# Performance work log

Hardware: AMD Instinct MI355X
Metric: run time of the kernel (lower is better)

The kernel has to match this reference:

```python
import jax, jax.numpy as jnp
import numpy as np

N, E, C_IN, C_OUT = 50000, 800000, 64, 64
BN_EPS = 1e-5


def _batchnorm(h, gamma, beta):
    # Training-mode BatchNorm1d: batch statistics over dim 0, biased variance.
    mean = h.mean(axis=0)
    var = h.var(axis=0)  # ddof=0, matches PyTorch normalization stats
    return gamma * (h - mean) * jax.lax.rsqrt(var + BN_EPS) + beta


def setup_inputs() -> dict:
    key = jax.random.key(0)
    ks = jax.random.split(key, 6)
    x = jax.random.normal(ks[0], (N, C_IN), dtype=jnp.float32)
    edge_index = jax.random.randint(ks[1], (2, E), 0, N, dtype=jnp.int32)
    edge_weight = jax.random.uniform(ks[2], (E,), dtype=jnp.float32)
    s1 = 1.0 / np.sqrt(C_IN).astype(np.float32)
    s2 = 1.0 / np.sqrt(2 * C_IN).astype(np.float32)
    pool_W = jax.random.uniform(ks[3], (C_IN, C_IN), jnp.float32, -s1, s1)
    pool_b = jnp.zeros((C_IN,), jnp.float32)
    final_W = jax.random.uniform(ks[4], (2 * C_IN, C_OUT), jnp.float32, -s2, s2)
    final_b = jnp.zeros((C_OUT,), jnp.float32)
    return {
        "x": x,
        "edge_index": edge_index,
        "edge_weight": edge_weight,
        "pool_W": pool_W,
        "pool_b": pool_b,
        "bn_pool_gamma": jnp.ones((C_IN,), jnp.float32),
        "bn_pool_beta": jnp.zeros((C_IN,), jnp.float32),
        "final_W": final_W,
        "final_b": final_b,
        "bn_final_gamma": jnp.ones((C_OUT,), jnp.float32),
        "bn_final_beta": jnp.zeros((C_OUT,), jnp.float32),
        "coef": jnp.float32(0.5),
    }


def reference(x, edge_index, edge_weight, pool_W, pool_b, bn_pool_gamma,
              bn_pool_beta, final_W, final_b, bn_final_gamma, bn_final_beta,
              coef):
    src, dst = edge_index[0], edge_index[1]
    # gather src node features, scale by edge weight  -> [E, C_IN]
    edge_feat = x[src] * (1.0 + coef * edge_weight[:, None])
    pooled = edge_feat @ pool_W + pool_b              # [E, C_IN]
    pooled = jax.nn.relu(_batchnorm(pooled, bn_pool_gamma, bn_pool_beta))
    # scatter-max into destination nodes; empty segments -> 0 (pooled >= 0)
    agg = jax.ops.segment_max(pooled, dst, num_segments=x.shape[0])
    agg = jnp.maximum(agg, 0.0)                       # fill -inf (empty) with 0
    h = jnp.concatenate([x, agg], axis=-1) @ final_W + final_b  # [N, C_OUT]
    h = _batchnorm(h, bn_final_gamma, bn_final_beta)
    return jax.nn.relu(h)
```

## Files before the change

### kernel.cpp

```cpp
#include <hip/hip_runtime.h>
#include <hip/hip_fp16.h>
#include <math.h>
#include <float.h>

#define BN_EPS 1e-5f
#define SLOTS 64
#define SB 256


typedef __attribute__((ext_vector_type(8))) short bf16x8;
typedef __attribute__((ext_vector_type(4))) float f32x4;

__device__ inline unsigned short f2bf(float f) {
    unsigned u = __float_as_uint(f);
    return (unsigned short)((u + 0x7fffu + ((u >> 16) & 1u)) >> 16);
}
__device__ inline float bf2f(unsigned short h) {
    return __uint_as_float(((unsigned)h) << 16);
}

__global__ __launch_bounds__(256, 4) void k_scatter_gemm(
        const int* __restrict__ src, const int* __restrict__ dst,
        const float* __restrict__ w, const float* __restrict__ coef_p,
        int* __restrict__ cnt, unsigned* __restrict__ csr, int E,
        const float* __restrict__ x, const float* __restrict__ W,
        unsigned short* __restrict__ ybf, int nrows, int gemmGrid) {
    __shared__ unsigned short Wt[64 * 72];
    if (blockIdx.x < SB) {
        const float coef = *coef_p;
        const int tid = blockIdx.x * 256 + threadIdx.x;
        const int stride4 = SB * 256 * 4;
        for (int base = tid * 4; base < E; base += stride4) {
            if (base + 3 < E) {
                int4   s4 = *(const int4*)(src + base);
                int4   d4 = *(const int4*)(dst + base);
                float4 w4 = *(const float4*)(w + base);
                int sn[4] = {s4.x, s4.y, s4.z, s4.w};
                int dn[4] = {d4.x, d4.y, d4.z, d4.w};
                float wv[4] = {w4.x, w4.y, w4.z, w4.w};
                unsigned hs[4];
                int pos[4];
#pragma unroll
                for (int j = 0; j < 4; ++j) {
                    float s = fmaf(coef, wv[j], 1.0f);
                    hs[j] = (unsigned)__half_as_ushort(__float2half(s));
                    pos[j] = atomicAdd(&cnt[dn[j]], 1);
                }
#pragma unroll
                for (int j = 0; j < 4; ++j)
                    if (pos[j] < SLOTS)
                        csr[(size_t)dn[j] * SLOTS + pos[j]] =
                            ((unsigned)sn[j] << 16) | hs[j];
            } else {
                for (int i = base; i < E; ++i) {
                    int sn = src[i], tn = dst[i];
                    float s = fmaf(coef, w[i], 1.0f);
                    unsigned hs = (unsigned)__half_as_ushort(__float2half(s));
                    int pos = atomicAdd(&cnt[tn], 1);
                    if (pos < SLOTS)
                        csr[(size_t)tn * SLOTS + pos] = ((unsigned)sn << 16) | hs;
                }
            }
        }
        return;
    }
    const int bid = blockIdx.x - SB;
    for (int i = threadIdx.x; i < 64 * 64; i += 256) {
        int k = i >> 6, n = i & 63;
        Wt[n * 72 + k] = f2bf(W[i]);
    }
    __syncthreads();
    const int lane = threadIdx.x & 63;
    const int wave = threadIdx.x >> 6;
    const int quad = lane >> 4;
    const int ln = lane & 15;
    bf16x8 Bf[2][4];
#pragma unroll
    for (int kc = 0; kc < 2; ++kc)
#pragma unroll
        for (int ct = 0; ct < 4; ++ct)
            Bf[kc][ct] = *(const bf16x8*)&Wt[(ct * 16 + ln) * 72 + kc * 32 + quad * 8];
    const int T = (nrows + 15) >> 4;
    const int gw = bid * 4 + wave;
    const int nw = gemmGrid * 4;
    for (int t = gw; t < T; t += nw) {
        const int row = t * 16 + ln;
        bf16x8 af[2];
        if (row < nrows) {
            const float* xr = x + (size_t)row * 64;
#pragma unroll
            for (int kc = 0; kc < 2; ++kc) {
                float4 p = *(const float4*)(xr + kc * 32 + quad * 8);
                float4 q = *(const float4*)(xr + kc * 32 + quad * 8 + 4);
                bf16x8 a;
                a[0] = (short)f2bf(p.x); a[1] = (short)f2bf(p.y);
                a[2] = (short)f2bf(p.z); a[3] = (short)f2bf(p.w);
                a[4] = (short)f2bf(q.x); a[5] = (short)f2bf(q.y);
                a[6] = (short)f2bf(q.z); a[7] = (short)f2bf(q.w);
                af[kc] = a;
            }
        } else {
            bf16x8 z;
#pragma unroll
            for (int j = 0; j < 8; ++j) z[j] = 0;
            af[0] = z; af[1] = z;
        }
        f32x4 acc[4];
#pragma unroll
        for (int ct = 0; ct < 4; ++ct) { acc[ct][0]=0.f; acc[ct][1]=0.f; acc[ct][2]=0.f; acc[ct][3]=0.f; }
#pragma unroll
        for (int ct = 0; ct < 4; ++ct) {
            acc[ct] = __builtin_amdgcn_mfma_f32_16x16x32_bf16(af[0], Bf[0][ct], acc[ct], 0, 0, 0);
            acc[ct] = __builtin_amdgcn_mfma_f32_16x16x32_bf16(af[1], Bf[1][ct], acc[ct], 0, 0, 0);
        }
#pragma unroll
        for (int r = 0; r < 4; ++r) {
            int ro = t * 16 + quad * 4 + r;
            if (ro < nrows) {
#pragma unroll
                for (int ct = 0; ct < 4; ++ct)
                    ybf[(size_t)ro * 64 + ct * 16 + ln] = f2bf(acc[ct][r]);
            }
        }
    }
}

__global__ __launch_bounds__(256) void k_gather_max(const unsigned short* __restrict__ ybf,
                             const unsigned* __restrict__ csr, const int* __restrict__ cnt,
                             float* __restrict__ M, float* __restrict__ partials, int nrows) {
    int t = blockIdx.x * blockDim.x + threadIdx.x;
    int node = t >> 4;
    int sub = threadIdx.x & 15;
    int rg = threadIdx.x >> 4;
    int c0 = sub * 4;
    size_t base = (size_t)node * SLOTS;
    int dg = 0;
    if (node < nrows) { dg = cnt[node]; if (dg > SLOTS) dg = SLOTS; }
    float m0 = -FLT_MAX, m1 = -FLT_MAX, m2 = -FLT_MAX, m3 = -FLT_MAX;
    float s1[4] = {0, 0, 0, 0}, s2[4] = {0, 0, 0, 0};
    for (int k0 = 0; k0 < dg; k0 += 16) {
        int kk = k0 + sub;
        unsigned pk = (kk < dg) ? csr[base + kk] : 0u;
        int cnt16 = dg - k0; if (cnt16 > 16) cnt16 = 16;
        if (cnt16 == 16) {
            ushort4 uv[16];
            float sv[16];
#pragma unroll
            for (int j = 0; j < 16; ++j) {
                unsigned r = (unsigned)__shfl((int)pk, j, 16);
                sv[j] = __half2float(__ushort_as_half((unsigned short)(r & 0xffffu)));
                uv[j] = *(const ushort4*)&ybf[(size_t)(r >> 16) * 64 + c0];
            }
#pragma unroll
            for (int j = 0; j < 16; ++j) {
                float v0 = sv[j] * bf2f(uv[j].x), v1 = sv[j] * bf2f(uv[j].y);
                float v2 = sv[j] * bf2f(uv[j].z), v3 = sv[j] * bf2f(uv[j].w);
                m0 = fmaxf(m0, v0); s1[0] += v0; s2[0] = fmaf(v0, v0, s2[0]);
                m1 = fmaxf(m1, v1); s1[1] += v1; s2[1] = fmaf(v1, v1, s2[1]);
                m2 = fmaxf(m2, v2); s1[2] += v2; s2[2] = fmaf(v2, v2, s2[2]);
                m3 = fmaxf(m3, v3); s1[3] += v3; s2[3] = fmaf(v3, v3, s2[3]);
            }
        } else {
            for (int j = 0; j < cnt16; ++j) {
                unsigned r = (unsigned)__shfl((int)pk, j, 16);
                int sn = r >> 16;
                float sv = __half2float(__ushort_as_half((unsigned short)(r & 0xffffu)));
                ushort4 uv = *(const ushort4*)&ybf[(size_t)sn * 64 + c0];
                float v0 = sv * bf2f(uv.x), v1 = sv * bf2f(uv.y);
                float v2 = sv * bf2f(uv.z), v3 = sv * bf2f(uv.w);
                m0 = fmaxf(m0, v0); s1[0] += v0; s2[0] = fmaf(v0, v0, s2[0]);
                m1 = fmaxf(m1, v1); s1[1] += v1; s2[1] = fmaf(v1, v1, s2[1]);
                m2 = fmaxf(m2, v2); s1[2] += v2; s2[2] = fmaf(v2, v2, s2[2]);
                m3 = fmaxf(m3, v3); s1[3] += v3; s2[3] = fmaf(v3, v3, s2[3]);
            }
        }
    }
    if (node < nrows)
        *(float4*)&M[(size_t)node * 64 + c0] = make_float4(m0, m1, m2, m3);
    __shared__ float red[16][68];
#pragma unroll
    for (int j = 0; j < 4; ++j) red[rg][c0 + j] = s1[j];
    __syncthreads();
    if (rg == 0) {
#pragma unroll
        for (int j = 0; j < 4; ++j) {
            float tt = 0.0f;
            for (int r = 0; r < 16; ++r) tt += red[r][c0 + j];
            partials[(size_t)blockIdx.x * 128 + c0 + j] = tt;
        }
    }
    __syncthreads();
#pragma unroll
    for (int j = 0; j < 4; ++j) red[rg][c0 + j] = s2[j];
    __syncthreads();
    if (rg == 0) {
#pragma unroll
        for (int j = 0; j < 4; ++j) {
            float tt = 0.0f;
            for (int r = 0; r < 16; ++r) tt += red[r][c0 + j];
            partials[(size_t)blockIdx.x * 128 + 64 + c0 + j] = tt;
        }
    }
}

__global__ __launch_bounds__(256) void k_red1(const float* __restrict__ partials, int P,
                                              float* __restrict__ p2) {
    int c = threadIdx.x & 127;
    int half = threadIdx.x >> 7;
    float acc = 0.0f;
    for (int r = blockIdx.x * 2 + half; r < P; r += 256)
        acc += partials[(size_t)r * 128 + c];
    __shared__ float sh[256];
    sh[threadIdx.x] = acc;
    __syncthreads();
    if (half == 0) p2[(size_t)blockIdx.x * 128 + c] = sh[c] + sh[128 + c];
}

__global__ __launch_bounds__(1024) void k_red2(const float* __restrict__ p2,
                             const float* __restrict__ pool_b, const float* __restrict__ gamma,
                             const float* __restrict__ beta, float invE,
                             float* __restrict__ coef) {
    int c = threadIdx.x & 127;
    int seg = threadIdx.x >> 7;
    float acc = 0.0f;
    for (int r = seg; r < 128; r += 8) acc += p2[(size_t)r * 128 + c];
    __shared__ float red[8][128];
    red[seg][c] = acc;
    __syncthreads();
    if (seg == 0) {
        float tt = 0.0f;
#pragma unroll
        for (int s = 0; s < 8; ++s) tt += red[s][c];
        red[0][c] = tt;
    }
    __syncthreads();
    if (threadIdx.x < 64) {
        int c0 = threadIdx.x;
        float S1 = red[0][c0], S2 = red[0][64 + c0];
        float s1 = S1 * invE;
        float b = pool_b[c0];
        float mean = s1 + b;
        float ex2 = S2 * invE + 2.0f * b * s1 + b * b;
        float var = ex2 - mean * mean;
        float a = gamma[c0] * rsqrtf(var + BN_EPS);
        coef[c0] = a;
        coef[64 + c0] = beta[c0] - a * s1;
    }
}

__global__ __launch_bounds__(1024) void k_red2f(const float* __restrict__ p2,
                             const float* __restrict__ gamma, const float* __restrict__ beta,
                             float invN, float* __restrict__ coef) {
    int c = threadIdx.x & 127;
    int seg = threadIdx.x >> 7;
    float acc = 0.0f;
    for (int r = seg; r < 128; r += 8) acc += p2[(size_t)r * 128 + c];
    __shared__ float red[8][128];
    red[seg][c] = acc;
    __syncthreads();
    if (seg == 0) {
        float tt = 0.0f;
#pragma unroll
        for (int s = 0; s < 8; ++s) tt += red[s][c];
        red[0][c] = tt;
    }
    __syncthreads();
    if (threadIdx.x < 64) {
        int c0 = threadIdx.x;
        float mean = red[0][c0] * invN;
        float var = red[0][64 + c0] * invN - mean * mean;
        float a = gamma[c0] * rsqrtf(var + BN_EPS);
        coef[c0] = a;
        coef[64 + c0] = beta[c0] - a * mean;
    }
}

__global__ __launch_bounds__(256, 2) void k_final_gemm(const float* __restrict__ x,
                             const float* __restrict__ M, const float* __restrict__ coef,
                             const float* __restrict__ W, const float* __restrict__ b,
                             float* __restrict__ h, float* __restrict__ partials, int nrows) {
    __shared__ unsigned short Wt[64 * 136];
    __shared__ float hp[128];
    for (int i = threadIdx.x; i < 128 * 64; i += 256) {
        int k = i >> 6, n = i & 63;
        Wt[n * 136 + k] = f2bf(W[i]);
    }
    if (threadIdx.x < 128) hp[threadIdx.x] = 0.0f;
    __syncthreads();
    const int lane = threadIdx.x & 63;
    const int wave = threadIdx.x >> 6;
    const int quad = lane >> 4;
    const int ln = lane & 15;
    bf16x8 Bf[4][4];
#pragma unroll
    for (int kc = 0; kc < 4; ++kc)
#pragma unroll
        for (int ct = 0; ct < 4; ++ct)
            Bf[kc][ct] = *(const bf16x8*)&Wt[(ct * 16 + ln) * 136 + kc * 32 + quad * 8];
    float bias[4];
#pragma unroll
    for (int ct = 0; ct < 4; ++ct) bias[ct] = b[ct * 16 + ln];
    float ca[2][8], cd[2][8];
#pragma unroll
    for (int g = 0; g < 2; ++g) {
        int ch = g * 32 + quad * 8;
#pragma unroll
        for (int j = 0; j < 8; ++j) {
            ca[g][j] = coef[ch + j];
            cd[g][j] = coef[64 + ch + j];
        }
    }
    float ls1[4] = {0, 0, 0, 0}, ls2[4] = {0, 0, 0, 0};
    const int T = (nrows + 15) >> 4;
    const int gw = blockIdx.x * 4 + wave;
    const int nw = gridDim.x * 4;
    for (int t = gw; t < T; t += nw) {
        const int row = t * 16 + ln;
        bf16x8 af[4];
        if (row < nrows) {
            const float* xr = x + (size_t)row * 64;
#pragma unroll
            for (int kc = 0; kc < 2; ++kc) {
                float4 p = *(const float4*)(xr + kc * 32 + quad * 8);
                float4 q = *(const float4*)(xr + kc * 32 + quad * 8 + 4);
                bf16x8 a;
                a[0] = (short)f2bf(p.x); a[1] = (short)f2bf(p.y);
                a[2] = (short)f2bf(p.z); a[3] = (short)f2bf(p.w);
                a[4] = (short)f2bf(q.x); a[5] = (short)f2bf(q.y);
                a[6] = (short)f2bf(q.z); a[7] = (short)f2bf(q.w);
                af[kc] = a;
            }
            const float* mr = M + (size_t)row * 64;
#pragma unroll
            for (int g = 0; g < 2; ++g) {
                const float* mp = mr + g * 32 + quad * 8;
                float4 p = *(const float4*)mp;
                float4 q = *(const float4*)(mp + 4);
                float v[8] = {p.x, p.y, p.z, p.w, q.x, q.y, q.z, q.w};
                bf16x8 a;
#pragma unroll
                for (int j = 0; j < 8; ++j)
                    a[j] = (short)f2bf(fmaxf(fmaf(ca[g][j], v[j], cd[g][j]), 0.0f));
                af[2 + g] = a;
            }
        } else {
            bf16x8 z;
#pragma unroll
            for (int j = 0; j < 8; ++j) z[j] = 0;
#pragma unroll
            for (int kc = 0; kc < 4; ++kc) af[kc] = z;
        }
        f32x4 acc[4];
#pragma unroll
        for (int ct = 0; ct < 4; ++ct) { acc[ct][0]=0.f; acc[ct][1]=0.f; acc[ct][2]=0.f; acc[ct][3]=0.f; }
#pragma unroll
        for (int kc = 0; kc < 4; ++kc)
#pragma unroll
            for (int ct = 0; ct < 4; ++ct)
                acc[ct] = __builtin_amdgcn_mfma_f32_16x16x32_bf16(af[kc], Bf[kc][ct], acc[ct], 0, 0, 0);
#pragma unroll
        for (int r = 0; r < 4; ++r) {
            int ro = t * 16 + quad * 4 + r;
            if (ro < nrows) {
#pragma unroll
                for (int ct = 0; ct < 4; ++ct) {
                    float hv = acc[ct][r] + bias[ct];
                    h[(size_t)ro * 64 + ct * 16 + ln] = hv;
                    ls1[ct] += hv;
                    ls2[ct] = fmaf(hv, hv, ls2[ct]);
                }
            }
        }
    }
#pragma unroll
    for (int ct = 0; ct < 4; ++ct) {
        atomicAdd(&hp[ct * 16 + ln], ls1[ct]);
        atomicAdd(&hp[64 + ct * 16 + ln], ls2[ct]);
    }
    __syncthreads();
    if (threadIdx.x < 128)
        partials[(size_t)blockIdx.x * 128 + threadIdx.x] = hp[threadIdx.x];
}

__global__ __launch_bounds__(256) void k_bn_out(const float* __restrict__ h,
                         const float* __restrict__ coef,
                         float* __restrict__ out, int nrows) {
    const int idx = blockIdx.x * blockDim.x + threadIdx.x;
    const int total = nrows * 16;
    if (idx >= total) return;
    const int c0 = (idx & 15) * 4;
    const float4 hv = *(const float4*)(h + (size_t)idx * 4);
    float4 o;
    float* op = (float*)&o;
    const float* hp = (const float*)&hv;
#pragma unroll
    for (int j = 0; j < 4; ++j) {
        const int c = c0 + j;
        op[j] = fmaxf(fmaf(coef[c], hp[j], coef[64 + c]), 0.0f);
    }
    *(float4*)(out + (size_t)idx * 4) = o;
}

extern "C" void kernel_launch(void* const* d_in, const int* in_sizes, int n_in,
                              void* d_out, int out_size, void* d_ws, size_t ws_size,
                              hipStream_t stream) {
    const float* x       = (const float*)d_in[0];
    const int*   eidx    = (const int*)d_in[1];
    const float* ew      = (const float*)d_in[2];
    const float* pool_W  = (const float*)d_in[3];
    const float* pool_b  = (const float*)d_in[4];
    const float* g1      = (const float*)d_in[5];
    const float* b1      = (const float*)d_in[6];
    const float* final_W = (const float*)d_in[7];
    const float* final_b = (const float*)d_in[8];
    const float* g2      = (const float*)d_in[9];
    const float* b2      = (const float*)d_in[10];
    const float* coef    = (const float*)d_in[11];

    const int N = in_sizes[0] / 64;
    const int E = in_sizes[1] / 2;
    const int* src = eidx;
    const int* dst = eidx + E;

    const int PG  = (N * 16 + 255) / 256;
    const int T   = (N + 15) / 16;
    const int nbT = (T + 3) / 4;

    unsigned* ws = (unsigned*)d_ws;
    int*   cnt      = (int*)ws;
    float* bncoef   = (float*)(ws + (size_t)N);
    float* coef2    = (float*)(ws + (size_t)N + 128);
    float* p2       = (float*)(ws + (size_t)N + 256);
    float* p2F      = p2 + 16384;
    float* partialsG= p2F + 16384;
    float* partialsF= partialsG + (size_t)PG * 128;
    unsigned short* ybf = (unsigned short*)(partialsF + (size_t)nbT * 128);
    unsigned* csrF  = (unsigned*)ybf + (size_t)32 * N;
    float* M        = (float*)(csrF + (size_t)SLOTS * N);

    hipMemsetAsync(cnt, 0, (size_t)N * 4, stream);

    k_scatter_gemm<<<SB + nbT, 256, 0, stream>>>(src, dst, ew, coef, cnt, csrF, E,
                                                 x, pool_W, ybf, N, nbT);
    k_gather_max<<<PG, 256, 0, stream>>>(ybf, csrF, cnt, M, partialsG, N);
    k_red1   <<<128, 256, 0, stream>>>(partialsG, PG, p2);
    k_red2   <<<1, 1024, 0, stream>>>(p2, pool_b, g1, b1, 1.0f / (float)E, bncoef);
    k_final_gemm<<<nbT, 256, 0, stream>>>(x, M, bncoef, final_W, final_b,
                                          (float*)d_out, partialsF, N);
    k_red1   <<<128, 256, 0, stream>>>(partialsF, nbT, p2F);
    k_red2f  <<<1, 1024, 0, stream>>>(p2F, g2, b2, 1.0f / (float)N, coef2);
    k_bn_out <<<(N * 16 + 255) / 256, 256, 0, stream>>>((const float*)d_out, coef2,
                                                        (float*)d_out, N);
}
```

Before: 216.9 us.

## Partition CSR scatter blocks by destination range to localize atomics

Splits the SB scatter blocks into 8 groups, each owning one eighth of the destination-node range. Every group reads the full edge list but only does the atomic count and CSR write for edges whose dst falls in its range. The aim is to keep each group's atomics and CSR writes in a smaller region of memory, which may improve cache or L2 locality (possibly per-XCD on MI355X). The cost is that each edge is read 8 times, and the per-edge branch adds divergence.

```diff
diff --git a/kernel.cpp b/kernel.cpp
--- a/kernel.cpp
+++ b/kernel.cpp
@@ -28,9 +28,13 @@
     __shared__ unsigned short Wt[64 * 72];
     if (blockIdx.x < SB) {
         const float coef = *coef_p;
-        const int tid = blockIdx.x * 256 + threadIdx.x;
-        const int stride4 = SB * 256 * 4;
-        for (int base = tid * 4; base < E; base += stride4) {
+        const int r  = blockIdx.x & 7;
+        const int lo = (int)(((long long)nrows * r) >> 3);
+        const int hi = (int)(((long long)nrows * (r + 1)) >> 3);
+        const int pb  = blockIdx.x >> 3;
+        const int tid = pb * 256 + threadIdx.x;
+        const int PT  = (SB >> 3) * 256;
+        for (int base = tid * 4; base < E; base += PT * 4) {
             if (base + 3 < E) {
                 int4   s4 = *(const int4*)(src + base);
                 int4   d4 = *(const int4*)(dst + base);
@@ -38,27 +42,28 @@
                 int sn[4] = {s4.x, s4.y, s4.z, s4.w};
                 int dn[4] = {d4.x, d4.y, d4.z, d4.w};
                 float wv[4] = {w4.x, w4.y, w4.z, w4.w};
-                unsigned hs[4];
-                int pos[4];
 #pragma unroll
                 for (int j = 0; j < 4; ++j) {
-                    float s = fmaf(coef, wv[j], 1.0f);
-                    hs[j] = (unsigned)__half_as_ushort(__float2half(s));
-                    pos[j] = atomicAdd(&cnt[dn[j]], 1);
+                    if (dn[j] >= lo && dn[j] < hi) {
+                        float s = fmaf(coef, wv[j], 1.0f);
+                        unsigned hs = (unsigned)__half_as_ushort(__float2half(s));
+                        int pos = atomicAdd(&cnt[dn[j]], 1);
+                        if (pos < SLOTS)
+                            csr[(size_t)dn[j] * SLOTS + pos] =
+                                ((unsigned)sn[j] << 16) | hs;
+                    }
                 }
-#pragma unroll
-                for (int j = 0; j < 4; ++j)
-                    if (pos[j] < SLOTS)
-                        csr[(size_t)dn[j] * SLOTS + pos[j]] =
-                            ((unsigned)sn[j] << 16) | hs[j];
             } else {
                 for (int i = base; i < E; ++i) {
-                    int sn = src[i], tn = dst[i];
-                    float s = fmaf(coef, w[i], 1.0f);
-                    unsigned hs = (unsigned)__half_as_ushort(__float2half(s));
-                    int pos = atomicAdd(&cnt[tn], 1);
-                    if (pos < SLOTS)
-                        csr[(size_t)tn * SLOTS + pos] = ((unsigned)sn << 16) | hs;
+                    int tn = dst[i];
+                    if (tn >= lo && tn < hi) {
+                        int sn = src[i];
+                        float s = fmaf(coef, w[i], 1.0f);
+                        unsigned hs = (unsigned)__half_as_ushort(__float2half(s));
+                        int pos = atomicAdd(&cnt[tn], 1);
+                        if (pos < SLOTS)
+                            csr[(size_t)tn * SLOTS + pos] = ((unsigned)sn << 16) | hs;
+                    }
                 }
             }
         }
```

Result: slower. 241.6 us (+11.4%).
